# Performance work log

Measured on AMD Instinct MI355X. Metric: run time of the kernel, lower is better.

## Reference

```python
import jax, jax.numpy as jnp
import numpy as np

NEG_SLOPE = 0.2  # PyG GATConv default negative_slope
N_NODES = 4096
N_EDGES = 32768
IN_CH = 128
HID = 512
OUT_CH = 10
HEADS = 8


def gat_conv(x, src, dst, W, a_src, a_dst, bias, num_nodes):
    """PyG-style GATConv (eval mode, self-loops already in src/dst).
    x: [N, F_in], W: [F_in, H*C], a_src/a_dst: [H, C], bias: [H*C].
    Returns concat-heads output [N, H*C]."""
    H, C = a_src.shape
    h = (x @ W).reshape(num_nodes, H, C)                      # [N,H,C]
    alpha_src = jnp.sum(h * a_src, axis=-1)                   # [N,H]
    alpha_dst = jnp.sum(h * a_dst, axis=-1)                   # [N,H]
    e = alpha_src[src] + alpha_dst[dst]                       # [E,H] per-edge logits
    e = jnp.where(e > 0, e, NEG_SLOPE * e)                    # leaky_relu
    # segment softmax over incoming edges of each dst node (self-loops => non-empty)
    m = jax.ops.segment_max(e, dst, num_segments=num_nodes)   # [N,H]
    e = jnp.exp(e - m[dst])
    denom = jax.ops.segment_sum(e, dst, num_segments=num_nodes)
    alpha = e / denom[dst]                                    # [E,H]
    msg = h[src] * alpha[:, :, None]                          # [E,H,C] gather+weight
    out = jax.ops.segment_sum(msg, dst, num_segments=num_nodes)  # scatter-add
    return out.reshape(num_nodes, H * C) + bias


def setup_inputs() -> dict:
    key = jax.random.key(0)
    ks = jax.random.split(key, 16)
    s = 0.05
    inp = {
        "x": jax.random.normal(ks[0], (N_NODES, IN_CH), jnp.float32),
        "edge_index": jax.random.randint(ks[1], (2, N_EDGES), 0, N_NODES, jnp.int64),
        "edge_attr": jax.random.normal(ks[2], (N_EDGES, 16), jnp.float32),
        "W1": jax.random.normal(ks[3], (IN_CH, HEADS * HID), jnp.float32) * s,
        "a_src1": jax.random.normal(ks[4], (HEADS, HID), jnp.float32) * s,
        "a_dst1": jax.random.normal(ks[5], (HEADS, HID), jnp.float32) * s,
        "b1": jnp.zeros((HEADS * HID,), jnp.float32),
        "W2": jax.random.normal(ks[6], (HEADS * HID, HID), jnp.float32) * s,
        "a_src2": jax.random.normal(ks[7], (1, HID), jnp.float32) * s,
        "a_dst2": jax.random.normal(ks[8], (1, HID), jnp.float32) * s,
        "b2": jnp.zeros((HID,), jnp.float32),
        # MLP head
        "fc1_w": jax.random.normal(ks[9], (4096, 512), jnp.float32) * s,
        "fc1_b": jnp.zeros((512,), jnp.float32),
        "fc2_w": jax.random.normal(ks[10], (512, 128), jnp.float32) * s,
        "fc2_b": jnp.zeros((128,), jnp.float32),
        "fc3_w": jax.random.normal(ks[11], (128, OUT_CH), jnp.float32) * s,
        "fc3_b": jnp.zeros((OUT_CH,), jnp.float32),
    }
    return inp


def reference(x, edge_index, edge_attr, W1, a_src1, a_dst1, b1, W2, a_src2, a_dst2, b2,
              fc1_w, fc1_b, fc2_w, fc2_b, fc3_w, fc3_b):
    # edge_attr is ignored: GATConv was built without edge_dim (lin_edge is None in PyG).
    del edge_attr
    n = x.shape[0]
    loops = jnp.arange(n, dtype=edge_index.dtype)
    src = jnp.concatenate([edge_index[0], loops])  # add_self_loops=True default
    dst = jnp.concatenate([edge_index[1], loops])
    h = jax.nn.relu(gat_conv(x, src, dst, W1, a_src1, a_dst1, b1, n))   # [N, 4096]
    h = jax.nn.relu(gat_conv(h, src, dst, W2, a_src2, a_dst2, b2, n))   # [N, 512]
    g = h.reshape(-1, 8 * h.shape[-1])                                   # [N/8, 4096]
    g = jax.nn.relu(g @ fc1_w + fc1_b)
    g = jax.nn.relu(g @ fc2_w + fc2_b)
    return g @ fc3_w + fc3_b                                             # [N/8, 10]
```

## Files before the change

### kernel.cpp

```cpp
#include <hip/hip_runtime.h>
#include <cstdint>
#include <cstddef>

#define NN    4096
#define E0C   32768
#define ETC   (E0C+NN)
#define HC1   8
#define CC    512
#define F_IN  128
#define NEG_SLOPE_F 0.2f
#define ELLW  64

typedef __bf16 bf16_t;
typedef __bf16 bf16x8 __attribute__((ext_vector_type(8)));
typedef __bf16 bf16x4 __attribute__((ext_vector_type(4)));
typedef float  f32x4  __attribute__((ext_vector_type(4)));

__device__ __forceinline__ void tcast_body(const float* __restrict__ W, bf16_t* __restrict__ Wt,
                                           int K, int N, int bx, int by)
{
    __shared__ float t[32][33];
    int bn = bx * 32, bk = by * 32;
    int tx = threadIdx.x & 31, ty = threadIdx.x >> 5;
    #pragma unroll
    for (int i = 0; i < 32; i += 8)
        t[ty + i][tx] = W[(size_t)(bk + ty + i) * N + bn + tx];
    __syncthreads();
    #pragma unroll
    for (int i = 0; i < 32; i += 8)
        Wt[(size_t)(bn + ty + i) * K + bk + tx] = (bf16_t)t[tx][ty + i];
}

__global__ __launch_bounds__(256) void prep_k(const float* __restrict__ x,
    const float* __restrict__ W1, const float* __restrict__ W2,
    const float* __restrict__ fc1w, const float* __restrict__ a_src1,
    const float* __restrict__ a_dst1, const int* __restrict__ ei,
    bf16_t* __restrict__ x_bf, bf16_t* __restrict__ Wt1, bf16_t* __restrict__ Wt2,
    bf16_t* __restrict__ fc1wt, bf16_t* __restrict__ w1sT,
    int* __restrict__ srcELL, int* __restrict__ indeg)
{
    const int b = blockIdx.x;
    if (b < 512) {
        int i = (b * 256 + threadIdx.x) * 4;
        float4 v = *(const float4*)&x[i];
        bf16x4 o;
        o[0] = (bf16_t)v.x; o[1] = (bf16_t)v.y; o[2] = (bf16_t)v.z; o[3] = (bf16_t)v.w;
        *(bf16x4*)&x_bf[i] = o;
    } else if (b < 1024) {
        int bl = b - 512;
        tcast_body(W1, Wt1, F_IN, 4096, bl % 128, bl / 128);
    } else if (b < 3072) {
        int bl = b - 1024;
        tcast_body(W2, Wt2, 4096, 512, bl % 16, bl / 16);
    } else if (b < 5120) {
        int bl = b - 3072;
        tcast_body(fc1w, fc1wt, 4096, 512, bl % 16, bl / 16);
    } else if (b < 5152) {
        int bl = b - 5120;
        int wave = threadIdx.x >> 6, lane = threadIdx.x & 63;
        int k = bl * 4 + wave;
        int hd = lane >> 3;
        int co = (lane & 7) * 64;
        const float* wrow = W1 + (size_t)k * (HC1 * CC) + hd * CC + co;
        const float* vs = a_src1 + hd * CC + co;
        const float* vd = a_dst1 + hd * CC + co;
        float s = 0.f, d = 0.f;
        #pragma unroll 4
        for (int t = 0; t < 64; ++t) {
            float w = wrow[t];
            s += w * vs[t];
            d += w * vd[t];
        }
        #pragma unroll
        for (int off = 1; off < 8; off <<= 1) {
            s += __shfl_xor(s, off);
            d += __shfl_xor(d, off);
        }
        if ((lane & 7) == 0) {
            w1sT[hd * F_IN + k]       = (bf16_t)s;
            w1sT[(hd + 8) * F_IN + k] = (bf16_t)d;
        }
    } else {
        int e = (b - 5152) * 256 + threadIdx.x;
        if (e < ETC) {
            int s, d;
            if (e < E0C) { s = ei[e]; d = ei[E0C + e]; }
            else         { s = e - E0C; d = s; }
            int pos = atomicAdd(&indeg[d], 1);
            if (pos < ELLW) srcELL[d * ELLW + pos] = s;
        }
    }
}

__global__ __launch_bounds__(256, 2) void gemm1_alpha_k(const bf16_t* __restrict__ A,
    const bf16_t* __restrict__ Bt, bf16_t* __restrict__ C,
    const bf16_t* __restrict__ w1sT, float* __restrict__ as1, float* __restrict__ ad1)
{
    __shared__ bf16_t As[128 * 32];
    __shared__ bf16_t Bs[128 * 32];
    const int b = blockIdx.x;
    const int tid = threadIdx.x;
    const int wave = tid >> 6, lane = tid & 63;
    const int lm = lane & 15, quad = lane >> 4;

    if (b < 1024) {
        const int bm = (b & 31) * 128, bn = (b >> 5) * 128;
        const int wm = wave >> 1, wn = wave & 1;
        const int sr = tid >> 2;
        const int kg = tid & 3;
        const int swz = ((kg ^ (sr & 3)) * 8);

        const bf16_t* Aptr = A + (size_t)(bm + sr) * F_IN + kg * 8;
        const bf16_t* Bptr = Bt + (size_t)(bn + sr) * F_IN + kg * 8;
        const size_t rowskip = (size_t)64 * F_IN;

        bf16x8 ra0 = *(const bf16x8*)(Aptr);
        bf16x8 ra1 = *(const bf16x8*)(Aptr + rowskip);
        bf16x8 rb0 = *(const bf16x8*)(Bptr);
        bf16x8 rb1 = *(const bf16x8*)(Bptr + rowskip);

        f32x4 acc[4][4] = {};

        for (int k0 = 0; k0 < F_IN; k0 += 32) {
            __syncthreads();
            *(bf16x8*)&As[sr * 32 + swz]        = ra0;
            *(bf16x8*)&As[(sr + 64) * 32 + swz] = ra1;
            *(bf16x8*)&Bs[sr * 32 + swz]        = rb0;
            *(bf16x8*)&Bs[(sr + 64) * 32 + swz] = rb1;
            __syncthreads();
            if (k0 + 32 < F_IN) {
                Aptr += 32; Bptr += 32;
                ra0 = *(const bf16x8*)(Aptr);
                ra1 = *(const bf16x8*)(Aptr + rowskip);
                rb0 = *(const bf16x8*)(Bptr);
                rb1 = *(const bf16x8*)(Bptr + rowskip);
            }
            const int fswz = ((quad ^ (lm & 3)) * 8);
            bf16x8 af[4], bfr[4];
            #pragma unroll
            for (int i = 0; i < 4; ++i) {
                af[i]  = *(const bf16x8*)&As[(wm * 64 + i * 16 + lm) * 32 + fswz];
                bfr[i] = *(const bf16x8*)&Bs[(wn * 64 + i * 16 + lm) * 32 + fswz];
            }
            #pragma unroll
            for (int mt = 0; mt < 4; ++mt)
                #pragma unroll
                for (int nt = 0; nt < 4; ++nt)
                    acc[mt][nt] = __builtin_amdgcn_mfma_f32_16x16x32_bf16(af[mt], bfr[nt], acc[mt][nt], 0, 0, 0);
        }
        #pragma unroll
        for (int nt = 0; nt < 4; ++nt) {
            int gc = bn + wn * 64 + nt * 16 + lm;
            #pragma unroll
            for (int mt = 0; mt < 4; ++mt)
                #pragma unroll
                for (int r = 0; r < 4; ++r) {
                    int gr = bm + wm * 64 + mt * 16 + quad * 4 + r;
                    C[(size_t)gr * 4096 + gc] = (bf16_t)acc[mt][nt][r];
                }
        }
    } else {
        const int bm = (b - 1024) * 64 + wave * 16;
        f32x4 acc = {};
        #pragma unroll
        for (int k0 = 0; k0 < F_IN; k0 += 32) {
            bf16x8 af = *(const bf16x8*)&A[(size_t)(bm + lm) * F_IN + k0 + quad * 8];
            bf16x8 bf = *(const bf16x8*)&w1sT[lm * F_IN + k0 + quad * 8];
            acc = __builtin_amdgcn_mfma_f32_16x16x32_bf16(af, bf, acc, 0, 0, 0);
        }
        #pragma unroll
        for (int r = 0; r < 4; ++r) {
            int n = bm + quad * 4 + r;
            if (lm < 8) as1[n * HC1 + lm] = acc[r];
            else        ad1[n * HC1 + (lm - 8)] = acc[r];
        }
    }
}

__global__ __launch_bounds__(256, 2) void gemm128s_k(const bf16_t* __restrict__ A,
                                                     const bf16_t* __restrict__ Bt,
                                                     float* __restrict__ Cpart,
                                                     int M, int N, int K, int Kc)
{
    __shared__ bf16_t As[128 * 32];
    __shared__ bf16_t Bs[128 * 32];
    const int tid = threadIdx.x;
    const int bm = blockIdx.x * 128, bn = blockIdx.y * 128;
    const int kz = blockIdx.z;
    const int k_beg = kz * Kc;
    const int k_end = k_beg + Kc;

    const int wave = tid >> 6, lane = tid & 63;
    const int wm = wave >> 1, wn = wave & 1;
    const int lm = lane & 15, quad = lane >> 4;

    const int sr = tid >> 2;
    const int kg = tid & 3;
    const int swz = ((kg ^ (sr & 3)) * 8);

    const bf16_t* Aptr = A + (size_t)(bm + sr) * K + k_beg + kg * 8;
    const bf16_t* Bptr = Bt + (size_t)(bn + sr) * K + k_beg + kg * 8;
    const size_t rowskip = (size_t)64 * K;

    bf16x8 ra0 = *(const bf16x8*)(Aptr);
    bf16x8 ra1 = *(const bf16x8*)(Aptr + rowskip);
    bf16x8 rb0 = *(const bf16x8*)(Bptr);
    bf16x8 rb1 = *(const bf16x8*)(Bptr + rowskip);

    f32x4 acc[4][4] = {};

    for (int k0 = k_beg; k0 < k_end; k0 += 32) {
        __syncthreads();
        *(bf16x8*)&As[sr * 32 + swz]        = ra0;
        *(bf16x8*)&As[(sr + 64) * 32 + swz] = ra1;
        *(bf16x8*)&Bs[sr * 32 + swz]        = rb0;
        *(bf16x8*)&Bs[(sr + 64) * 32 + swz] = rb1;
        __syncthreads();
        if (k0 + 32 < k_end) {
            Aptr += 32; Bptr += 32;
            ra0 = *(const bf16x8*)(Aptr);
            ra1 = *(const bf16x8*)(Aptr + rowskip);
            rb0 = *(const bf16x8*)(Bptr);
            rb1 = *(const bf16x8*)(Bptr + rowskip);
        }
        const int fswz = ((quad ^ (lm & 3)) * 8);
        bf16x8 af[4], bfr[4];
        #pragma unroll
        for (int i = 0; i < 4; ++i) {
            af[i]  = *(const bf16x8*)&As[(wm * 64 + i * 16 + lm) * 32 + fswz];
            bfr[i] = *(const bf16x8*)&Bs[(wn * 64 + i * 16 + lm) * 32 + fswz];
        }
        #pragma unroll
        for (int mt = 0; mt < 4; ++mt)
            #pragma unroll
            for (int nt = 0; nt < 4; ++nt)
                acc[mt][nt] = __builtin_amdgcn_mfma_f32_16x16x32_bf16(af[mt], bfr[nt], acc[mt][nt], 0, 0, 0);
    }

    float* P = Cpart + (size_t)kz * M * N;
    #pragma unroll
    for (int nt = 0; nt < 4; ++nt) {
        int gc = bn + wn * 64 + nt * 16 + lm;
        #pragma unroll
        for (int mt = 0; mt < 4; ++mt)
            #pragma unroll
            for (int r = 0; r < 4; ++r) {
                int gr = bm + wm * 64 + mt * 16 + quad * 4 + r;
                P[(size_t)gr * N + gc] = acc[mt][nt][r];
            }
    }
}

__global__ __launch_bounds__(256) void reduce_h2_k(const float* __restrict__ P,
    const float* __restrict__ a_s, const float* __restrict__ a_d,
    bf16_t* __restrict__ h2bf, float* __restrict__ as2, float* __restrict__ ad2)
{
    const int t = threadIdx.x;
    const int i = (blockIdx.x * 256 + t) * 4;
    f32x4 s = *(const f32x4*)&P[i];
    #pragma unroll
    for (int z = 1; z < 4; ++z)
        s += *(const f32x4*)&P[(size_t)z * NN * CC + i];
    bf16x4 o;
    #pragma unroll
    for (int j = 0; j < 4; ++j) o[j] = (bf16_t)s[j];
    *(bf16x4*)&h2bf[i] = o;
    const int c = i & (CC - 1);
    const int row = i >> 9;
    f32x4 va = *(const f32x4*)&a_s[c];
    f32x4 vd = *(const f32x4*)&a_d[c];
    float ls = s[0]*va[0] + s[1]*va[1] + s[2]*va[2] + s[3]*va[3];
    float ld = s[0]*vd[0] + s[1]*vd[1] + s[2]*vd[2] + s[3]*vd[3];
    #pragma unroll
    for (int off = 32; off > 0; off >>= 1) {
        ls += __shfl_down(ls, off);
        ld += __shfl_down(ld, off);
    }
    if ((t & 63) == 0) {
        atomicAdd(&as2[row], ls);
        atomicAdd(&ad2[row], ld);
    }
}

__global__ __launch_bounds__(128) void tail_k(const float* __restrict__ P,
                                              const float* __restrict__ fc1b,
                                              const float* __restrict__ fc2w,
                                              const float* __restrict__ fc2b,
                                              const float* __restrict__ fc3w,
                                              const float* __restrict__ fc3b,
                                              float* __restrict__ out)
{
    __shared__ float sA[512];
    __shared__ float sF2[128];
    const int m = blockIdx.x, t = threadIdx.x;
    const int MN = 512 * 512;
    #pragma unroll
    for (int i = 0; i < 4; ++i) {
        int c = t + i * 128;
        float v = 0.f;
        #pragma unroll
        for (int z = 0; z < 16; ++z)
            v += P[(size_t)z * MN + (size_t)m * 512 + c];
        sA[c] = fmaxf(v + fc1b[c], 0.f);
    }
    __syncthreads();
    float a0 = 0.f, a1 = 0.f, a2 = 0.f, a3 = 0.f;
    #pragma unroll 4
    for (int k = 0; k < 512; k += 4) {
        a0 += sA[k + 0] * fc2w[(k + 0) * 128 + t];
        a1 += sA[k + 1] * fc2w[(k + 1) * 128 + t];
        a2 += sA[k + 2] * fc2w[(k + 2) * 128 + t];
        a3 += sA[k + 3] * fc2w[(k + 3) * 128 + t];
    }
    sF2[t] = fmaxf((a0 + a1) + (a2 + a3) + fc2b[t], 0.f);
    __syncthreads();
    if (t < 10) {
        float o = fc3b[t];
        #pragma unroll 4
        for (int k = 0; k < 128; ++k)
            o += sF2[k] * fc3w[k * 10 + t];
        out[(size_t)m * 10 + t] = o;
    }
}

template<int H>
__global__ __launch_bounds__(256) void aggregate_k(const bf16_t* __restrict__ hbuf,
    const float* __restrict__ as, const float* __restrict__ ad,
    const int* __restrict__ indeg, const int* __restrict__ srcELL,
    const float* __restrict__ bias, bf16_t* __restrict__ outb)
{
    const int b = blockIdx.x;
    const int hd = b % H;
    const int g  = b / H;
    const int wave = threadIdx.x >> 6, lane = threadIdx.x & 63;
    const int n = g * 4 + wave;
    const int c = lane * 8;

    const int deg = min(indeg[n], ELLW);
    const float adn = ad[n * H + hd];

    int vsrc = 0; float vp = 0.f;
    if (lane < deg) {
        vsrc = srcELL[n * ELLW + lane];
        float v = as[vsrc * H + hd] + adn;
        v = (v > 0.f) ? v : NEG_SLOPE_F * v;
        vp = __expf(v);
    }
    float denom = vp;
    #pragma unroll
    for (int off = 1; off < 64; off <<= 1)
        denom += __shfl_xor(denom, off);
    vp *= 1.f / denom;

    float acc[8] = {};
    int ii = 0;
    for (; ii + 4 <= deg; ii += 4) {
        int s0 = __shfl(vsrc, ii),     s1 = __shfl(vsrc, ii + 1);
        int s2 = __shfl(vsrc, ii + 2), s3 = __shfl(vsrc, ii + 3);
        float a0 = __shfl(vp, ii),     a1 = __shfl(vp, ii + 1);
        float a2 = __shfl(vp, ii + 2), a3 = __shfl(vp, ii + 3);
        bf16x8 r0 = *(const bf16x8*)&hbuf[((size_t)s0 * H + hd) * CC + c];
        bf16x8 r1 = *(const bf16x8*)&hbuf[((size_t)s1 * H + hd) * CC + c];
        bf16x8 r2 = *(const bf16x8*)&hbuf[((size_t)s2 * H + hd) * CC + c];
        bf16x8 r3 = *(const bf16x8*)&hbuf[((size_t)s3 * H + hd) * CC + c];
        #pragma unroll
        for (int j = 0; j < 8; ++j) {
            acc[j] += a0 * (float)r0[j];
            acc[j] += a1 * (float)r1[j];
            acc[j] += a2 * (float)r2[j];
            acc[j] += a3 * (float)r3[j];
        }
    }
    for (; ii < deg; ++ii) {
        int s = __shfl(vsrc, ii);
        float al = __shfl(vp, ii);
        bf16x8 rv = *(const bf16x8*)&hbuf[((size_t)s * H + hd) * CC + c];
        #pragma unroll
        for (int j = 0; j < 8; ++j)
            acc[j] += al * (float)rv[j];
    }
    size_t ob = ((size_t)n * H + hd) * CC;
    bf16x8 o;
    #pragma unroll
    for (int j = 0; j < 8; ++j)
        o[j] = (bf16_t)fmaxf(acc[j] + bias[hd * CC + c + j], 0.f);
    *(bf16x8*)&outb[ob + c] = o;
}

extern "C" void kernel_launch(void* const* d_in, const int* in_sizes, int n_in,
                              void* d_out, int out_size, void* d_ws, size_t ws_size,
                              hipStream_t stream) {
    const float* x      = (const float*)d_in[0];
    const int*   ei     = (const int*)d_in[1];
    const float* W1     = (const float*)d_in[3];
    const float* a_src1 = (const float*)d_in[4];
    const float* a_dst1 = (const float*)d_in[5];
    const float* b1     = (const float*)d_in[6];
    const float* W2     = (const float*)d_in[7];
    const float* a_src2 = (const float*)d_in[8];
    const float* a_dst2 = (const float*)d_in[9];
    const float* b2     = (const float*)d_in[10];
    const float* fc1w   = (const float*)d_in[11];
    const float* fc1b   = (const float*)d_in[12];
    const float* fc2w   = (const float*)d_in[13];
    const float* fc2b   = (const float*)d_in[14];
    const float* fc3w   = (const float*)d_in[15];
    const float* fc3b   = (const float*)d_in[16];
    float* out = (float*)d_out;

    char* ws = (char*)d_ws;
    size_t o = 0;
    auto take = [&](size_t bytes) -> char* {
        char* p = ws + o;
        o = (o + bytes + 255) & ~(size_t)255;
        return p;
    };
    int*    indeg  = (int*)take(NN * 4);
    float*  as2    = (float*)take(NN * 4);
    float*  ad2    = (float*)take(NN * 4);
    size_t zero_bytes = o;
    int*    srcELL = (int*)take((size_t)NN * ELLW * 4);
    float*  as1    = (float*)take((size_t)NN * HC1 * 4);
    float*  ad1    = (float*)take((size_t)NN * HC1 * 4);
    bf16_t* w1sT   = (bf16_t*)take((size_t)16 * F_IN * 2);
    bf16_t* x_bf   = (bf16_t*)take((size_t)NN * F_IN * 2);
    bf16_t* Wt1    = (bf16_t*)take((size_t)F_IN * 4096 * 2);
    bf16_t* Wt2    = (bf16_t*)take((size_t)4096 * 512 * 2);
    bf16_t* fc1wt  = (bf16_t*)take((size_t)4096 * 512 * 2);
    bf16_t* h1bf   = (bf16_t*)take((size_t)NN * 4096 * 2);
    bf16_t* out1bf = (bf16_t*)take((size_t)NN * 4096 * 2);
    bf16_t* h2bf   = (bf16_t*)take((size_t)NN * 512 * 2);
    bf16_t* out2bf = (bf16_t*)take((size_t)NN * 512 * 2);
    float*  part   = (float*)take((size_t)4 * NN * 512 * 4);

    hipMemsetAsync(d_ws, 0, zero_bytes, stream);

    prep_k<<<dim3(5296), dim3(256), 0, stream>>>(x, W1, W2, fc1w, a_src1, a_dst1, ei,
                                                 x_bf, Wt1, Wt2, fc1wt, w1sT,
                                                 srcELL, indeg);

    gemm1_alpha_k<<<dim3(1088), dim3(256), 0, stream>>>(
        x_bf, Wt1, h1bf, w1sT, as1, ad1);
    aggregate_k<HC1><<<dim3(NN / 4 * HC1), dim3(256), 0, stream>>>(
        h1bf, as1, ad1, indeg, srcELL, b1, out1bf);

    gemm128s_k<<<dim3(32, 4, 4), dim3(256), 0, stream>>>(
        out1bf, Wt2, part, 4096, 512, 4096, 1024);
    reduce_h2_k<<<dim3(NN * 512 / 1024), dim3(256), 0, stream>>>(
        part, a_src2, a_dst2, h2bf, as2, ad2);
    aggregate_k<1><<<dim3(NN / 4), dim3(256), 0, stream>>>(
        h2bf, as2, ad2, indeg, srcELL, b2, out2bf);

    gemm128s_k<<<dim3(4, 4, 16), dim3(256), 0, stream>>>(
        out2bf, fc1wt, part, 512, 512, 4096, 256);
    tail_k<<<dim3(512), dim3(128), 0, stream>>>(
        part, fc1b, fc2w, fc2b, fc3w, fc3b, out);
}
```

Baseline: 221.3 us.

## Aggregate raw features before layer-1 projection to avoid gathering wide hidden rows

Layer 1 is reordered: attention weights are computed first, neighbour inputs are aggregated per head in the 128-wide input space (xagg), and a per-head GEMM then projects the aggregated features with bias and ReLU fused in. This removes the write and the gather of the 4096-wide h1 buffer. The cost is a new NN×8×128 intermediate and a GEMM whose A operand is strided per head. Rounding changes slightly because aggregation now happens before the projection, in bf16.

```diff
diff --git a/kernel.cpp b/kernel.cpp
--- a/kernel.cpp
+++ b/kernel.cpp
@@ -14,6 +14,7 @@
 typedef __bf16 bf16_t;
 typedef __bf16 bf16x8 __attribute__((ext_vector_type(8)));
 typedef __bf16 bf16x4 __attribute__((ext_vector_type(4)));
+typedef __bf16 bf16x2 __attribute__((ext_vector_type(2)));
 typedef float  f32x4  __attribute__((ext_vector_type(4)));
 
 __device__ __forceinline__ void tcast_body(const float* __restrict__ W, bf16_t* __restrict__ Wt,
@@ -92,88 +93,149 @@
     }
 }
 
-__global__ __launch_bounds__(256, 2) void gemm1_alpha_k(const bf16_t* __restrict__ A,
-    const bf16_t* __restrict__ Bt, bf16_t* __restrict__ C,
-    const bf16_t* __restrict__ w1sT, float* __restrict__ as1, float* __restrict__ ad1)
+__global__ __launch_bounds__(256) void alpha1_k(const bf16_t* __restrict__ x_bf,
+                                                const bf16_t* __restrict__ w1sT,
+                                                float* __restrict__ as1, float* __restrict__ ad1)
+{
+    const int wave = threadIdx.x >> 6, lane = threadIdx.x & 63;
+    const int bm = blockIdx.x * 64 + wave * 16;
+    const int lm = lane & 15, quad = lane >> 4;
+    f32x4 acc = {};
+    #pragma unroll
+    for (int k0 = 0; k0 < F_IN; k0 += 32) {
+        bf16x8 af = *(const bf16x8*)&x_bf[(size_t)(bm + lm) * F_IN + k0 + quad * 8];
+        bf16x8 bf = *(const bf16x8*)&w1sT[lm * F_IN + k0 + quad * 8];
+        acc = __builtin_amdgcn_mfma_f32_16x16x32_bf16(af, bf, acc, 0, 0, 0);
+    }
+    #pragma unroll
+    for (int r = 0; r < 4; ++r) {
+        int n = bm + quad * 4 + r;
+        if (lm < 8) as1[n * HC1 + lm] = acc[r];
+        else        ad1[n * HC1 + (lm - 8)] = acc[r];
+    }
+}
+
+__global__ __launch_bounds__(256) void aggx_k(const bf16_t* __restrict__ x_bf,
+    const float* __restrict__ as1, const float* __restrict__ ad1,
+    const int* __restrict__ indeg, const int* __restrict__ srcELL,
+    bf16_t* __restrict__ xagg)
+{
+    const int wave = threadIdx.x >> 6, lane = threadIdx.x & 63;
+    const int n = blockIdx.x * 4 + wave;
+    const int c = lane * 2;
+    const int deg = min(indeg[n], ELLW);
+
+    int vsrc = 0;
+    float vp[HC1] = {};
+    if (lane < deg) {
+        vsrc = srcELL[n * ELLW + lane];
+        #pragma unroll
+        for (int hd = 0; hd < HC1; ++hd) {
+            float v = as1[vsrc * HC1 + hd] + ad1[n * HC1 + hd];
+            v = (v > 0.f) ? v : NEG_SLOPE_F * v;
+            vp[hd] = __expf(v);
+        }
+    }
+    #pragma unroll
+    for (int hd = 0; hd < HC1; ++hd) {
+        float dsum = vp[hd];
+        #pragma unroll
+        for (int off = 1; off < 64; off <<= 1)
+            dsum += __shfl_xor(dsum, off);
+        vp[hd] *= 1.f / dsum;
+    }
+
+    float acc[HC1][2] = {};
+    for (int ii = 0; ii < deg; ++ii) {
+        int s = __shfl(vsrc, ii);
+        bf16x2 rv = *(const bf16x2*)&x_bf[(size_t)s * F_IN + c];
+        float r0 = (float)rv[0], r1 = (float)rv[1];
+        #pragma unroll
+        for (int hd = 0; hd < HC1; ++hd) {
+            float al = __shfl(vp[hd], ii);
+            acc[hd][0] += al * r0;
+            acc[hd][1] += al * r1;
+        }
+    }
+    #pragma unroll
+    for (int hd = 0; hd < HC1; ++hd) {
+        bf16x2 o;
+        o[0] = (bf16_t)acc[hd][0];
+        o[1] = (bf16_t)acc[hd][1];
+        *(bf16x2*)&xagg[((size_t)n * HC1 + hd) * F_IN + c] = o;
+    }
+}
+
+__global__ __launch_bounds__(256, 2) void gemmh_k(const bf16_t* __restrict__ xagg,
+                                                  const bf16_t* __restrict__ Wt1,
+                                                  const float* __restrict__ b1,
+                                                  bf16_t* __restrict__ out1)
 {
     __shared__ bf16_t As[128 * 32];
     __shared__ bf16_t Bs[128 * 32];
-    const int b = blockIdx.x;
     const int tid = threadIdx.x;
+    const int bm = blockIdx.x * 128, bn = blockIdx.y * 128;
+    const int hd = blockIdx.z;
+
     const int wave = tid >> 6, lane = tid & 63;
+    const int wm = wave >> 1, wn = wave & 1;
     const int lm = lane & 15, quad = lane >> 4;
 
-    if (b < 1024) {
-        const int bm = (b & 31) * 128, bn = (b >> 5) * 128;
-        const int wm = wave >> 1, wn = wave & 1;
-        const int sr = tid >> 2;
-        const int kg = tid & 3;
-        const int swz = ((kg ^ (sr & 3)) * 8);
-
-        const bf16_t* Aptr = A + (size_t)(bm + sr) * F_IN + kg * 8;
-        const bf16_t* Bptr = Bt + (size_t)(bn + sr) * F_IN + kg * 8;
-        const size_t rowskip = (size_t)64 * F_IN;
-
-        bf16x8 ra0 = *(const bf16x8*)(Aptr);
-        bf16x8 ra1 = *(const bf16x8*)(Aptr + rowskip);
-        bf16x8 rb0 = *(const bf16x8*)(Bptr);
-        bf16x8 rb1 = *(const bf16x8*)(Bptr + rowskip);
-
-        f32x4 acc[4][4] = {};
-
-        for (int k0 = 0; k0 < F_IN; k0 += 32) {
-            __syncthreads();
-            *(bf16x8*)&As[sr * 32 + swz]        = ra0;
-            *(bf16x8*)&As[(sr + 64) * 32 + swz] = ra1;
-            *(bf16x8*)&Bs[sr * 32 + swz]        = rb0;
-            *(bf16x8*)&Bs[(sr + 64) * 32 + swz] = rb1;
-            __syncthreads();
-            if (k0 + 32 < F_IN) {
-                Aptr += 32; Bptr += 32;
-                ra0 = *(const bf16x8*)(Aptr);
-                ra1 = *(const bf16x8*)(Aptr + rowskip);
-                rb0 = *(const bf16x8*)(Bptr);
-                rb1 = *(const bf16x8*)(Bptr + rowskip);
+    const int sr = tid >> 2;
+    const int kg = tid & 3;
+    const int swz = ((kg ^ (sr & 3)) * 8);
+
+    const bf16_t* Aptr = xagg + ((size_t)(bm + sr) * HC1 + hd) * F_IN + kg * 8;
+    const bf16_t* Bptr = Wt1 + (size_t)(hd * CC + bn + sr) * F_IN + kg * 8;
+    const size_t raskip = (size_t)64 * HC1 * F_IN;
+    const size_t rbskip = (size_t)64 * F_IN;
+
+    bf16x8 ra0 = *(const bf16x8*)(Aptr);
+    bf16x8 ra1 = *(const bf16x8*)(Aptr + raskip);
+    bf16x8 rb0 = *(const bf16x8*)(Bptr);
+    bf16x8 rb1 = *(const bf16x8*)(Bptr + rbskip);
+
+    f32x4 acc[4][4] = {};
+
+    for (int k0 = 0; k0 < F_IN; k0 += 32) {
+        __syncthreads();
+        *(bf16x8*)&As[sr * 32 + swz]        = ra0;
+        *(bf16x8*)&As[(sr + 64) * 32 + swz] = ra1;
+        *(bf16x8*)&Bs[sr * 32 + swz]        = rb0;
+        *(bf16x8*)&Bs[(sr + 64) * 32 + swz] = rb1;
+        __syncthreads();
+        if (k0 + 32 < F_IN) {
+            Aptr += 32; Bptr += 32;
+            ra0 = *(const bf16x8*)(Aptr);
+            ra1 = *(const bf16x8*)(Aptr + raskip);
+            rb0 = *(const bf16x8*)(Bptr);
+            rb1 = *(const bf16x8*)(Bptr + rbskip);
+        }
+        const int fswz = ((quad ^ (lm & 3)) * 8);
+        bf16x8 af[4], bfr[4];
+        #pragma unroll
+        for (int i = 0; i < 4; ++i) {
+            af[i]  = *(const bf16x8*)&As[(wm * 64 + i * 16 + lm) * 32 + fswz];
+            bfr[i] = *(const bf16x8*)&Bs[(wn * 64 + i * 16 + lm) * 32 + fswz];
+        }
+        #pragma unroll
+        for (int mt = 0; mt < 4; ++mt)
+            #pragma unroll
+            for (int nt = 0; nt < 4; ++nt)
+                acc[mt][nt] = __builtin_amdgcn_mfma_f32_16x16x32_bf16(af[mt], bfr[nt], acc[mt][nt], 0, 0, 0);
+    }
+
+    #pragma unroll
+    for (int nt = 0; nt < 4; ++nt) {
+        int gc = bn + wn * 64 + nt * 16 + lm;
+        float bv = b1[hd * CC + gc];
+        #pragma unroll
+        for (int mt = 0; mt < 4; ++mt)
+            #pragma unroll
+            for (int r = 0; r < 4; ++r) {
+                int gr = bm + wm * 64 + mt * 16 + quad * 4 + r;
+                out1[(size_t)gr * 4096 + hd * CC + gc] = (bf16_t)fmaxf(acc[mt][nt][r] + bv, 0.f);
             }
-            const int fswz = ((quad ^ (lm & 3)) * 8);
-            bf16x8 af[4], bfr[4];
-            #pragma unroll
-            for (int i = 0; i < 4; ++i) {
-                af[i]  = *(const bf16x8*)&As[(wm * 64 + i * 16 + lm) * 32 + fswz];
-                bfr[i] = *(const bf16x8*)&Bs[(wn * 64 + i * 16 + lm) * 32 + fswz];
-            }
-            #pragma unroll
-            for (int mt = 0; mt < 4; ++mt)
-                #pragma unroll
-                for (int nt = 0; nt < 4; ++nt)
-                    acc[mt][nt] = __builtin_amdgcn_mfma_f32_16x16x32_bf16(af[mt], bfr[nt], acc[mt][nt], 0, 0, 0);
-        }
-        #pragma unroll
-        for (int nt = 0; nt < 4; ++nt) {
-            int gc = bn + wn * 64 + nt * 16 + lm;
-            #pragma unroll
-            for (int mt = 0; mt < 4; ++mt)
-                #pragma unroll
-                for (int r = 0; r < 4; ++r) {
-                    int gr = bm + wm * 64 + mt * 16 + quad * 4 + r;
-                    C[(size_t)gr * 4096 + gc] = (bf16_t)acc[mt][nt][r];
-                }
-        }
-    } else {
-        const int bm = (b - 1024) * 64 + wave * 16;
-        f32x4 acc = {};
-        #pragma unroll
-        for (int k0 = 0; k0 < F_IN; k0 += 32) {
-            bf16x8 af = *(const bf16x8*)&A[(size_t)(bm + lm) * F_IN + k0 + quad * 8];
-            bf16x8 bf = *(const bf16x8*)&w1sT[lm * F_IN + k0 + quad * 8];
-            acc = __builtin_amdgcn_mfma_f32_16x16x32_bf16(af, bf, acc, 0, 0, 0);
-        }
-        #pragma unroll
-        for (int r = 0; r < 4; ++r) {
-            int n = bm + quad * 4 + r;
-            if (lm < 8) as1[n * HC1 + lm] = acc[r];
-            else        ad1[n * HC1 + (lm - 8)] = acc[r];
-        }
     }
 }
 
@@ -323,26 +385,23 @@
     }
 }
 
-template<int H>
-__global__ __launch_bounds__(256) void aggregate_k(const bf16_t* __restrict__ hbuf,
+__global__ __launch_bounds__(256) void aggregate2_k(const bf16_t* __restrict__ hbuf,
     const float* __restrict__ as, const float* __restrict__ ad,
     const int* __restrict__ indeg, const int* __restrict__ srcELL,
     const float* __restrict__ bias, bf16_t* __restrict__ outb)
 {
-    const int b = blockIdx.x;
-    const int hd = b % H;
-    const int g  = b / H;
+    const int g = blockIdx.x;
     const int wave = threadIdx.x >> 6, lane = threadIdx.x & 63;
     const int n = g * 4 + wave;
     const int c = lane * 8;
 
     const int deg = min(indeg[n], ELLW);
-    const float adn = ad[n * H + hd];
+    const float adn = ad[n];
 
     int vsrc = 0; float vp = 0.f;
     if (lane < deg) {
         vsrc = srcELL[n * ELLW + lane];
-        float v = as[vsrc * H + hd] + adn;
+        float v = as[vsrc] + adn;
         v = (v > 0.f) ? v : NEG_SLOPE_F * v;
         vp = __expf(v);
     }
@@ -359,10 +418,10 @@
         int s2 = __shfl(vsrc, ii + 2), s3 = __shfl(vsrc, ii + 3);
         float a0 = __shfl(vp, ii),     a1 = __shfl(vp, ii + 1);
         float a2 = __shfl(vp, ii + 2), a3 = __shfl(vp, ii + 3);
-        bf16x8 r0 = *(const bf16x8*)&hbuf[((size_t)s0 * H + hd) * CC + c];
-        bf16x8 r1 = *(const bf16x8*)&hbuf[((size_t)s1 * H + hd) * CC + c];
-        bf16x8 r2 = *(const bf16x8*)&hbuf[((size_t)s2 * H + hd) * CC + c];
-        bf16x8 r3 = *(const bf16x8*)&hbuf[((size_t)s3 * H + hd) * CC + c];
+        bf16x8 r0 = *(const bf16x8*)&hbuf[(size_t)s0 * CC + c];
+        bf16x8 r1 = *(const bf16x8*)&hbuf[(size_t)s1 * CC + c];
+        bf16x8 r2 = *(const bf16x8*)&hbuf[(size_t)s2 * CC + c];
+        bf16x8 r3 = *(const bf16x8*)&hbuf[(size_t)s3 * CC + c];
         #pragma unroll
         for (int j = 0; j < 8; ++j) {
             acc[j] += a0 * (float)r0[j];
@@ -374,16 +433,16 @@
     for (; ii < deg; ++ii) {
         int s = __shfl(vsrc, ii);
         float al = __shfl(vp, ii);
-        bf16x8 rv = *(const bf16x8*)&hbuf[((size_t)s * H + hd) * CC + c];
+        bf16x8 rv = *(const bf16x8*)&hbuf[(size_t)s * CC + c];
         #pragma unroll
         for (int j = 0; j < 8; ++j)
             acc[j] += al * (float)rv[j];
     }
-    size_t ob = ((size_t)n * H + hd) * CC;
+    size_t ob = (size_t)n * CC;
     bf16x8 o;
     #pragma unroll
     for (int j = 0; j < 8; ++j)
-        o[j] = (bf16_t)fmaxf(acc[j] + bias[hd * CC + c + j], 0.f);
+        o[j] = (bf16_t)fmaxf(acc[j] + bias[c + j], 0.f);
     *(bf16x8*)&outb[ob + c] = o;
 }
 
@@ -424,10 +483,10 @@
     float*  ad1    = (float*)take((size_t)NN * HC1 * 4);
     bf16_t* w1sT   = (bf16_t*)take((size_t)16 * F_IN * 2);
     bf16_t* x_bf   = (bf16_t*)take((size_t)NN * F_IN * 2);
+    bf16_t* xagg   = (bf16_t*)take((size_t)NN * HC1 * F_IN * 2);
     bf16_t* Wt1    = (bf16_t*)take((size_t)F_IN * 4096 * 2);
     bf16_t* Wt2    = (bf16_t*)take((size_t)4096 * 512 * 2);
     bf16_t* fc1wt  = (bf16_t*)take((size_t)4096 * 512 * 2);
-    bf16_t* h1bf   = (bf16_t*)take((size_t)NN * 4096 * 2);
     bf16_t* out1bf = (bf16_t*)take((size_t)NN * 4096 * 2);
     bf16_t* h2bf   = (bf16_t*)take((size_t)NN * 512 * 2);
     bf16_t* out2bf = (bf16_t*)take((size_t)NN * 512 * 2);
@@ -439,16 +498,15 @@
                                                  x_bf, Wt1, Wt2, fc1wt, w1sT,
                                                  srcELL, indeg);
 
-    gemm1_alpha_k<<<dim3(1088), dim3(256), 0, stream>>>(
-        x_bf, Wt1, h1bf, w1sT, as1, ad1);
-    aggregate_k<HC1><<<dim3(NN / 4 * HC1), dim3(256), 0, stream>>>(
-        h1bf, as1, ad1, indeg, srcELL, b1, out1bf);
+    alpha1_k<<<dim3(64), dim3(256), 0, stream>>>(x_bf, w1sT, as1, ad1);
+    aggx_k<<<dim3(NN / 4), dim3(256), 0, stream>>>(x_bf, as1, ad1, indeg, srcELL, xagg);
+    gemmh_k<<<dim3(32, 4, 8), dim3(256), 0, stream>>>(xagg, Wt1, b1, out1bf);
 
     gemm128s_k<<<dim3(32, 4, 4), dim3(256), 0, stream>>>(
         out1bf, Wt2, part, 4096, 512, 4096, 1024);
     reduce_h2_k<<<dim3(NN * 512 / 1024), dim3(256), 0, stream>>>(
         part, a_src2, a_dst2, h2bf, as2, ad2);
-    aggregate_k<1><<<dim3(NN / 4), dim3(256), 0, stream>>>(
+    aggregate2_k<<<dim3(NN / 4), dim3(256), 0, stream>>>(
         h2bf, as2, ad2, indeg, srcELL, b2, out2bf);
 
     gemm128s_k<<<dim3(4, 4, 16), dim3(256), 0, stream>>>(
```

Result: faster. 211.1 us (-4.6%).
